# Performance work log

Measured on AMD Instinct MI355X. Metric: run time of the kernel, lower is better.

Reference implementation:

```python
import jax, jax.numpy as jnp
import numpy as np

D = 768; H = 12; DH = D // H; L = 12; FF = 3072; P = 20
IMG = (640, 360); NP_ = (IMG[0] // P) * (IMG[1] // P)  # 576 patches
NC = 10
EPS = 1e-5


def setup_inputs() -> dict:
    key = jax.random.key(0)
    ks = jax.random.split(key, 20)
    s = 0.02
    inp = {
        "x": jax.random.normal(ks[0], (16, 3, IMG[0], IMG[1]), jnp.float32),
        "patch_w": jax.random.normal(ks[1], (D, 3, P, P), jnp.float32) * s,
        "patch_b": jnp.zeros((D,), jnp.float32),
        "pos_emb": jax.random.normal(ks[2], (1, NP_, D), jnp.float32),
        "ln_g": jnp.ones((D,), jnp.float32),
        "ln_b": jnp.zeros((D,), jnp.float32),
        "Wq": jax.random.normal(ks[3], (L, D, D), jnp.float32) * s,
        "bq": jnp.zeros((L, D), jnp.float32),
        "Wk": jax.random.normal(ks[4], (L, D, D), jnp.float32) * s,
        "bk": jnp.zeros((L, D), jnp.float32),
        "Wv": jax.random.normal(ks[5], (L, D, D), jnp.float32) * s,
        "bv": jnp.zeros((L, D), jnp.float32),
        "Wo": jax.random.normal(ks[6], (L, D, D), jnp.float32) * s,
        "bo": jnp.zeros((L, D), jnp.float32),
        "W1": jax.random.normal(ks[7], (L, FF, D), jnp.float32) * s,
        "b1": jnp.zeros((L, FF), jnp.float32),
        "W2": jax.random.normal(ks[8], (L, D, FF), jnp.float32) * s,
        "b2": jnp.zeros((L, D), jnp.float32),
        "fc_w": jax.random.normal(ks[9], (NC, D), jnp.float32) * s,
        "fc_b": jnp.zeros((NC,), jnp.float32),
    }
    return inp


def _layer_norm(x, g, b):
    mu = jnp.mean(x, axis=-1, keepdims=True)
    var = jnp.mean(jnp.square(x - mu), axis=-1, keepdims=True)
    return (x - mu) * jax.lax.rsqrt(var + EPS) * g + b


def _forward(x, patch_w, patch_b, pos_emb, ln_g, ln_b,
             Wq, bq, Wk, bk, Wv, bv, Wo, bo, W1, b1, W2, b2, fc_w, fc_b):
    B = x.shape[0]
    Hp, Wp = IMG[0] // P, IMG[1] // P
    # patch embed: stride=kernel conv == per-patch linear
    patches = x.reshape(B, 3, Hp, P, Wp, P).transpose(0, 2, 4, 1, 3, 5)
    patches = patches.reshape(B, Hp * Wp, 3 * P * P)           # [B, N, 3*p*p]
    h = patches @ patch_w.reshape(D, -1).T + patch_b            # [B, N, D]
    h = h + pos_emb
    h = _layer_norm(h, ln_g, ln_b)

    def layer(h, p):
        wq, bq_, wk, bk_, wv, bv_, wo, bo_, w1, b1_, w2, b2_ = p
        N = h.shape[1]
        def heads(t):  # [B,N,D] -> [B,H,N,DH]
            return t.reshape(B, N, H, DH).transpose(0, 2, 1, 3)
        q = heads(h @ wq.T + bq_)
        k = heads(h @ wk.T + bk_)
        v = heads(h @ wv.T + bv_)
        scores = jnp.einsum('bhqd,bhkd->bhqk', q, k) / jnp.sqrt(jnp.float32(DH))
        attn = jax.nn.softmax(scores, axis=-1)
        o = jnp.einsum('bhqk,bhkd->bhqd', attn, v)
        o = o.transpose(0, 2, 1, 3).reshape(B, N, D) @ wo.T + bo_
        h = h + o
        ff = jax.nn.relu(h @ w1.T + b1_) @ w2.T + b2_
        return h + ff, None

    h, _ = jax.lax.scan(layer, h, (Wq, bq, Wk, bk, Wv, bv, Wo, bo, W1, b1, W2, b2))
    pooled = h.mean(axis=1)                                     # [B, D]
    return pooled @ fc_w.T + fc_b                               # [B, NC]


def reference(x, patch_w, patch_b, pos_emb, ln_g, ln_b,
              Wq, bq, Wk, bk, Wv, bv, Wo, bo, W1, b1, W2, b2, fc_w, fc_b):
    return _forward(x, patch_w, patch_b, pos_emb, ln_g, ln_b,
                    Wq, bq, Wk, bk, Wv, bv, Wo, bo, W1, b1, W2, b2, fc_w, fc_b)
```

## Files before the change

### kernel.cpp

```cpp
#include <hip/hip_runtime.h>
#include <stdint.h>
#include <stddef.h>

typedef __attribute__((ext_vector_type(8))) short short8;
typedef __attribute__((ext_vector_type(4))) float f32x4;

#define D_    768
#define HH    12
#define DHEAD 64
#define NP    576
#define BB    16
#define MROWS 9216
#define KPAT  1216
#define SCL   0.18033688011112042f

static __device__ __forceinline__ unsigned short f2bf(float f){
  union { float f; unsigned int u; } v; v.f = f;
  unsigned int u = v.u;
  return (unsigned short)((u + 0x7FFFu + ((u >> 16) & 1u)) >> 16);
}

static __device__ __forceinline__ void gld16(const void* g, void* l){
  __builtin_amdgcn_global_load_lds((const __attribute__((address_space(1))) void*)g,
                                   (__attribute__((address_space(3))) void*)l,
                                   16, 0, 0);
}

static __device__ __forceinline__ void barx(){
  asm volatile("" ::: "memory");
  __builtin_amdgcn_s_barrier();
  asm volatile("" ::: "memory");
}

template<int MF>
__global__ __launch_bounds__(512) void gemm8p(
    const unsigned short* __restrict__ A,
    const unsigned short* __restrict__ W,
    const float* __restrict__ bias,
    const float* __restrict__ pos,
    const float* res,
    float* outf,
    unsigned short* outb,
    int M, int N, int K, int relu)
{
  constexpr int BM = MF * 32;
  constexpr int NV = (MF == 8) ? 8 : 6;
  __shared__ unsigned short sA[4][BM*32];
  __shared__ unsigned short sB[4][256*32];

  const int NB = N >> 8;
  const int nwg = (int)gridDim.x;
  const int wid0 = (int)blockIdx.x;
  const int xcd = wid0 & 7, bidx = wid0 >> 3;
  const int q = nwg >> 3, r = nwg & 7;
  const int wid = (xcd < r ? xcd*(q+1) : r*(q+1) + (xcd-r)*q) + bidx;
  const int mb = wid / NB, nb = wid % NB;
  const int m0 = mb * BM, n0 = nb << 8;
  const int t = threadIdx.x;
  const int w = t >> 6, l = t & 63;
  const int wr = w >> 2, wc = w & 3;
  const int fr = l & 15, fq = l >> 4;

  const int srow = l >> 2;
  const int schk = (l & 3) ^ ((l >> 3) & 3);

  const f32x4 zero = {0.f, 0.f, 0.f, 0.f};
  f32x4 acc[MF][4];
  #pragma unroll
  for (int i = 0; i < MF; ++i)
    #pragma unroll
    for (int j = 0; j < 4; ++j) acc[i][j] = zero;

  const int KT = K >> 6;

  auto stgA = [&](int h){
    #pragma unroll
    for (int i = 0; i < BM/128; ++i){
      const int rb = i*128 + w*16;
      gld16(A + (size_t)(m0 + rb + srow) * K + (h<<5) + (schk<<3),
            &sA[h & 3][rb*32]);
    }
  };
  auto stgB = [&](int h){
    #pragma unroll
    for (int i = 0; i < 2; ++i){
      const int rb = i*128 + w*16;
      gld16(W + (size_t)(n0 + rb + srow) * K + (h<<5) + (schk<<3),
            &sB[h & 3][rb*32]);
    }
  };
  auto rdA = [&](short8* a, int slot, int mh){
    #pragma unroll
    for (int i = 0; i < MF/2; ++i){
      const int R = wr*(MF*16) + (mh*(MF/2) + i)*16 + fr;
      a[i] = *(const short8*)&sA[slot][R*32 + ((fq ^ ((R>>1)&3))<<3)];
    }
  };
  auto rdB = [&](short8* b, int slot){
    #pragma unroll
    for (int i = 0; i < 4; ++i){
      const int C = wc*64 + i*16 + fr;
      b[i] = *(const short8*)&sB[slot][C*32 + ((fq ^ ((C>>1)&3))<<3)];
    }
  };

  stgA(0); stgB(0); stgA(1); stgB(1); stgA(2); stgB(2);
  asm volatile("s_waitcnt vmcnt(%0)" :: "n"(NV) : "memory");
  barx();

  short8 a[MF/2], b[4];
  for (int kt = 0; kt < KT; ++kt){
    const int s0 = (2*kt) & 3, s1 = (2*kt+1) & 3;
    const int h3 = 2*kt + 3, h4 = 2*kt + 4;
    const bool g3 = h3 < 2*KT, g4 = h4 < 2*KT;
    const bool tail = kt >= KT - 2;

    rdA(a, s0, 0); rdB(b, s0);
    if (g3) stgA(h3);
    barx();
    __builtin_amdgcn_s_setprio(1);
    #pragma unroll
    for (int i = 0; i < MF/2; ++i)
      #pragma unroll
      for (int j = 0; j < 4; ++j)
        acc[i][j] = __builtin_amdgcn_mfma_f32_16x16x32_bf16(a[i], b[j], acc[i][j], 0, 0, 0);
    __builtin_amdgcn_s_setprio(0);
    barx();

    rdA(a, s0, 1);
    if (g3) stgB(h3);
    barx();
    __builtin_amdgcn_s_setprio(1);
    #pragma unroll
    for (int i = 0; i < MF/2; ++i)
      #pragma unroll
      for (int j = 0; j < 4; ++j)
        acc[MF/2 + i][j] = __builtin_amdgcn_mfma_f32_16x16x32_bf16(a[i], b[j], acc[MF/2 + i][j], 0, 0, 0);
    __builtin_amdgcn_s_setprio(0);
    if (tail) asm volatile("s_waitcnt vmcnt(0)" ::: "memory");
    else      asm volatile("s_waitcnt vmcnt(%0)" :: "n"(NV) : "memory");
    barx();

    rdA(a, s1, 0); rdB(b, s1);
    if (g4) stgA(h4);
    barx();
    __builtin_amdgcn_s_setprio(1);
    #pragma unroll
    for (int i = 0; i < MF/2; ++i)
      #pragma unroll
      for (int j = 0; j < 4; ++j)
        acc[i][j] = __builtin_amdgcn_mfma_f32_16x16x32_bf16(a[i], b[j], acc[i][j], 0, 0, 0);
    __builtin_amdgcn_s_setprio(0);
    barx();

    rdA(a, s1, 1);
    if (g4) stgB(h4);
    barx();
    __builtin_amdgcn_s_setprio(1);
    #pragma unroll
    for (int i = 0; i < MF/2; ++i)
      #pragma unroll
      for (int j = 0; j < 4; ++j)
        acc[MF/2 + i][j] = __builtin_amdgcn_mfma_f32_16x16x32_bf16(a[i], b[j], acc[MF/2 + i][j], 0, 0, 0);
    __builtin_amdgcn_s_setprio(0);
    if (tail) asm volatile("s_waitcnt vmcnt(0)" ::: "memory");
    else      asm volatile("s_waitcnt vmcnt(%0)" :: "n"(NV) : "memory");
    barx();
  }

  #pragma unroll
  for (int mf = 0; mf < MF; ++mf){
    #pragma unroll
    for (int nf = 0; nf < 4; ++nf){
      #pragma unroll
      for (int rr = 0; rr < 4; ++rr){
        const int row = m0 + wr*(MF*16) + mf*16 + (fq<<2) + rr;
        const int col = n0 + wc*64 + nf*16 + fr;
        float v = acc[mf][nf][rr] + bias[col];
        if (pos)  v += pos[(size_t)(row % NP) * D_ + col];
        if (res)  v += res[(size_t)row * N + col];
        if (relu) v = fmaxf(v, 0.f);
        const size_t idx = (size_t)row * N + col;
        if (outf) outf[idx] = v;
        if (outb) outb[idx] = f2bf(v);
      }
    }
  }
}

__global__ __launch_bounds__(512) void gemm4p(
    const unsigned short* __restrict__ A,
    const unsigned short* __restrict__ W,
    const float* __restrict__ bias,
    const float* __restrict__ pos,
    const float* res,
    float* outf,
    unsigned short* outb,
    int M, int N, int K, int relu)
{
  __shared__ unsigned short sA[4][128*32];
  __shared__ unsigned short sB[4][128*32];
  const int NB = N >> 7;
  const int nwg = (int)gridDim.x;
  const int wid0 = (int)blockIdx.x;
  const int xcd = wid0 & 7, bidx = wid0 >> 3;
  const int q = nwg >> 3, r = nwg & 7;
  const int wid = (xcd < r ? xcd*(q+1) : r*(q+1) + (xcd-r)*q) + bidx;
  const int mb = wid / NB, nb = wid % NB;
  const int m0 = mb << 7, n0 = nb << 7;
  const int t = threadIdx.x;
  const int w = t >> 6, l = t & 63;
  const int wr = w >> 1, wc = w & 1;
  const int fr = l & 15, fq = l >> 4;

  const int srow = l >> 2;
  const int schk = (l & 3) ^ ((l >> 3) & 3);

  const f32x4 zero = {0.f, 0.f, 0.f, 0.f};
  f32x4 acc[2][4];
  #pragma unroll
  for (int i = 0; i < 2; ++i)
    #pragma unroll
    for (int j = 0; j < 4; ++j) acc[i][j] = zero;

  const int P = K >> 5;

  auto stg = [&](int h){
    const int rb = w*16;
    gld16(A + (size_t)(m0 + rb + srow) * K + (h<<5) + (schk<<3), &sA[h & 3][rb*32]);
    gld16(W + (size_t)(n0 + rb + srow) * K + (h<<5) + (schk<<3), &sB[h & 3][rb*32]);
  };

  stg(0); stg(1); stg(2);
  asm volatile("s_waitcnt vmcnt(4)" ::: "memory");
  barx();

  short8 a[2], b[4];
  for (int p = 0; p < P; ++p){
    const int slot = p & 3;
    #pragma unroll
    for (int i = 0; i < 2; ++i){
      const int R = wr*32 + i*16 + fr;
      a[i] = *(const short8*)&sA[slot][R*32 + ((fq ^ ((R>>1)&3))<<3)];
    }
    #pragma unroll
    for (int i = 0; i < 4; ++i){
      const int C = wc*64 + i*16 + fr;
      b[i] = *(const short8*)&sB[slot][C*32 + ((fq ^ ((C>>1)&3))<<3)];
    }
    if (p + 3 < P) stg(p + 3);
    barx();
    __builtin_amdgcn_s_setprio(1);
    #pragma unroll
    for (int i = 0; i < 2; ++i)
      #pragma unroll
      for (int j = 0; j < 4; ++j)
        acc[i][j] = __builtin_amdgcn_mfma_f32_16x16x32_bf16(a[i], b[j], acc[i][j], 0, 0, 0);
    __builtin_amdgcn_s_setprio(0);
    if (p + 1 < P){
      if      (p <= P - 4) asm volatile("s_waitcnt vmcnt(4)" ::: "memory");
      else if (p == P - 3) asm volatile("s_waitcnt vmcnt(2)" ::: "memory");
      else                 asm volatile("s_waitcnt vmcnt(0)" ::: "memory");
      barx();
    }
  }

  #pragma unroll
  for (int mf = 0; mf < 2; ++mf){
    #pragma unroll
    for (int nf = 0; nf < 4; ++nf){
      #pragma unroll
      for (int rr = 0; rr < 4; ++rr){
        const int row = m0 + wr*32 + mf*16 + (fq<<2) + rr;
        const int col = n0 + wc*64 + nf*16 + fr;
        float v = acc[mf][nf][rr] + bias[col];
        if (pos)  v += pos[(size_t)(row % NP) * D_ + col];
        if (res)  v += res[(size_t)row * N + col];
        if (relu) v = fmaxf(v, 0.f);
        const size_t idx = (size_t)row * N + col;
        if (outf) outf[idx] = v;
        if (outb) outb[idx] = f2bf(v);
      }
    }
  }
}

__global__ __launch_bounds__(384) void k_attn(const unsigned short* __restrict__ qkv,
                                              unsigned short* __restrict__ o)
{
  __shared__ unsigned short Kl[2][32*64];
  __shared__ unsigned short Vt[2][64*64];
  const int nwg = (int)gridDim.x;
  int wid = (int)blockIdx.x;
  wid = (wid & 7) * (nwg >> 3) + (wid >> 3);
  const int bh = wid / 3, qs = wid % 3;
  const int b = bh / HH, h = bh % HH;
  const unsigned short* base = qkv + (size_t)b * NP * 2304 + h * DHEAD;
  const int t = threadIdx.x;
  const int w = t >> 6, l = t & 63;
  const int fr = l & 15, fq = l >> 4;
  const int sg = l & 7;
  const int sr = ((w & 3) << 3) + (l >> 3);
  const bool stw = (t < 256);

  short8 qfa[2], qfb[2];
  #pragma unroll
  for (int qt = 0; qt < 2; ++qt){
    const size_t qrow = (size_t)(qs*192 + (qt*6 + w)*16 + fr);
    qfa[qt] = *(const short8*)(base + qrow*2304 + (fq<<3));
    qfb[qt] = *(const short8*)(base + qrow*2304 + 32 + (fq<<3));
  }

  const f32x4 zero = {0.f, 0.f, 0.f, 0.f};
  float mx_[2] = {-1e30f, -1e30f};
  float ls_[2] = {0.f, 0.f};
  f32x4 oa[2][4];
  #pragma unroll
  for (int qt = 0; qt < 2; ++qt)
    #pragma unroll
    for (int nf = 0; nf < 4; ++nf) oa[qt][nf] = zero;

  if (stw){
    gld16(base + 768 + (size_t)sr*2304 + ((sg ^ (sr&7))<<3), &Kl[0][(w&3)*512]);
    short8 vv = *(const short8*)(base + 1536 + (size_t)sr*2304 + (sg<<3));
    asm volatile("s_waitcnt vmcnt(0)" ::: "memory");
    #pragma unroll
    for (int j = 0; j < 8; ++j){
      const int d = sg*8 + j;
      const int off = (d<<7) + ((((sr>>3) ^ j ^ sg) & 7) << 4) + ((sr&7)<<1);
      *(unsigned short*)((char*)&Vt[0][0] + off) = ((const unsigned short*)&vv)[j];
    }
  }
  __syncthreads();

  for (int kt = 0; kt < 18; ++kt){
    const int buf = kt & 1;
    short8 vv;
    const bool st = stw && (kt < 17);
    if (st){
      const int key = (kt+1)*32 + sr;
      gld16(base + 768 + (size_t)key*2304 + ((sg ^ (sr&7))<<3), &Kl[buf^1][(w&3)*512]);
      vv = *(const short8*)(base + 1536 + (size_t)key*2304 + (sg<<3));
    }

    const char* kb = (const char*)&Kl[buf][0];
    const int r0 = fr, r1 = 16 + fr;
    const short8 k00 = *(const short8*)(kb + (r0<<7) + (((fq    ) ^ (r0&7))<<4));
    const short8 k01 = *(const short8*)(kb + (r0<<7) + (((4+fq ) ^ (r0&7))<<4));
    const short8 k10 = *(const short8*)(kb + (r1<<7) + (((fq    ) ^ (r1&7))<<4));
    const short8 k11 = *(const short8*)(kb + (r1<<7) + (((4+fq ) ^ (r1&7))<<4));
    const char* vb = (const char*)&Vt[buf][0];

    #pragma unroll
    for (int qt = 0; qt < 2; ++qt){
      f32x4 s0 = zero, s1 = zero;
      s0 = __builtin_amdgcn_mfma_f32_16x16x32_bf16(k00, qfa[qt], s0, 0, 0, 0);
      s0 = __builtin_amdgcn_mfma_f32_16x16x32_bf16(k01, qfb[qt], s0, 0, 0, 0);
      s1 = __builtin_amdgcn_mfma_f32_16x16x32_bf16(k10, qfa[qt], s1, 0, 0, 0);
      s1 = __builtin_amdgcn_mfma_f32_16x16x32_bf16(k11, qfb[qt], s1, 0, 0, 0);
      float mx = fmaxf(fmaxf(fmaxf(s0[0], s0[1]), fmaxf(s0[2], s0[3])),
                       fmaxf(fmaxf(s1[0], s1[1]), fmaxf(s1[2], s1[3])));
      mx = fmaxf(mx, __shfl_xor(mx, 16));
      mx = fmaxf(mx, __shfl_xor(mx, 32));
      const float mn = fmaxf(mx_[qt], mx * SCL);
      const float fc = exp2f(mx_[qt] - mn);
      const float p0 = exp2f(s0[0]*SCL - mn), p1 = exp2f(s0[1]*SCL - mn);
      const float p2 = exp2f(s0[2]*SCL - mn), p3 = exp2f(s0[3]*SCL - mn);
      const float p4 = exp2f(s1[0]*SCL - mn), p5 = exp2f(s1[1]*SCL - mn);
      const float p6 = exp2f(s1[2]*SCL - mn), p7 = exp2f(s1[3]*SCL - mn);
      float ps = ((p0+p1)+(p2+p3)) + ((p4+p5)+(p6+p7));
      ps += __shfl_xor(ps, 16);
      ps += __shfl_xor(ps, 32);
      ls_[qt] = ls_[qt] * fc + ps;
      mx_[qt] = mn;
      if (!__all(fc == 1.0f)){
        const float fA = __shfl(fc, (fq<<2) + 0);
        const float fB = __shfl(fc, (fq<<2) + 1);
        const float fC = __shfl(fc, (fq<<2) + 2);
        const float fD = __shfl(fc, (fq<<2) + 3);
        #pragma unroll
        for (int nf = 0; nf < 4; ++nf){
          oa[qt][nf][0] *= fA; oa[qt][nf][1] *= fB;
          oa[qt][nf][2] *= fC; oa[qt][nf][3] *= fD;
        }
      }
      unsigned d0, d1, d2, d3;
      asm("v_cvt_pk_bf16_f32 %0, %1, %2" : "=v"(d0) : "v"(p0), "v"(p1));
      asm("v_cvt_pk_bf16_f32 %0, %1, %2" : "=v"(d1) : "v"(p2), "v"(p3));
      asm("v_cvt_pk_bf16_f32 %0, %1, %2" : "=v"(d2) : "v"(p4), "v"(p5));
      asm("v_cvt_pk_bf16_f32 %0, %1, %2" : "=v"(d3) : "v"(p6), "v"(p7));
      const int srcA = fr + ((fq & 1) << 5);
      const unsigned a0 = (unsigned)__shfl((int)d0, srcA);
      const unsigned a1 = (unsigned)__shfl((int)d1, srcA);
      const unsigned a2 = (unsigned)__shfl((int)d2, srcA);
      const unsigned a3 = (unsigned)__shfl((int)d3, srcA);
      const unsigned b0 = (unsigned)__shfl((int)d0, srcA + 16);
      const unsigned b1 = (unsigned)__shfl((int)d1, srcA + 16);
      const unsigned b2 = (unsigned)__shfl((int)d2, srcA + 16);
      const unsigned b3 = (unsigned)__shfl((int)d3, srcA + 16);
      const bool hi = fq >= 2;
      union { unsigned u[4]; short8 v; } pk;
      pk.u[0] = hi ? a2 : a0;
      pk.u[1] = hi ? a3 : a1;
      pk.u[2] = hi ? b2 : b0;
      pk.u[3] = hi ? b3 : b1;
      const short8 pa = pk.v;
      #pragma unroll
      for (int nf = 0; nf < 4; ++nf){
        const int d = (nf<<4) + fr;
        const short8 vf = *(const short8*)(vb + (d<<7) + (((fq ^ (d&7) ^ (d>>3)) & 7)<<4));
        oa[qt][nf] = __builtin_amdgcn_mfma_f32_16x16x32_bf16(pa, vf, oa[qt][nf], 0, 0, 0);
      }
    }

    if (st){
      asm volatile("s_waitcnt vmcnt(0)" ::: "memory");
      #pragma unroll
      for (int j = 0; j < 8; ++j){
        const int d = sg*8 + j;
        const int off = (d<<7) + ((((sr>>3) ^ j ^ sg) & 7) << 4) + ((sr&7)<<1);
        *(unsigned short*)((char*)&Vt[buf^1][0] + off) = ((const unsigned short*)&vv)[j];
      }
    }
    __syncthreads();
  }

  #pragma unroll
  for (int qt = 0; qt < 2; ++qt){
    const float rl = 1.f / ls_[qt];
    const float rA = __shfl(rl, (fq<<2)+0), rB = __shfl(rl, (fq<<2)+1);
    const float rC = __shfl(rl, (fq<<2)+2), rD = __shfl(rl, (fq<<2)+3);
    const size_t r0 = (size_t)(b*NP + qs*192 + (qt*6 + w)*16 + (fq<<2));
    #pragma unroll
    for (int nf = 0; nf < 4; ++nf){
      const int col = h*DHEAD + (nf<<4) + fr;
      o[(r0 + 0)*D_ + col] = f2bf(oa[qt][nf][0] * rA);
      o[(r0 + 1)*D_ + col] = f2bf(oa[qt][nf][1] * rB);
      o[(r0 + 2)*D_ + col] = f2bf(oa[qt][nf][2] * rC);
      o[(r0 + 3)*D_ + col] = f2bf(oa[qt][nf][3] * rD);
    }
  }
}

__global__ void k_f2b(const float* __restrict__ s, unsigned short* __restrict__ d, long n){
  long i = (long)blockIdx.x * blockDim.x + threadIdx.x;
  const long st = (long)gridDim.x * blockDim.x;
  for (; i < n; i += st) d[i] = f2bf(s[i]);
}

__global__ void k_pack_qkvw(const float* __restrict__ Wq, const float* __restrict__ Wk,
                            const float* __restrict__ Wv, unsigned short* __restrict__ dst){
  const long n = (long)12 * 2304 * 768;
  long i = (long)blockIdx.x * blockDim.x + threadIdx.x;
  const long st = (long)gridDim.x * blockDim.x;
  for (; i < n; i += st){
    const int lay = (int)(i / (2304 * 768));
    const int rem = (int)(i % (2304 * 768));
    const int r = rem / 768, k = rem % 768;
    const float* s = (r < 768) ? Wq : ((r < 1536) ? Wk : Wv);
    const int rr = (r < 768) ? r : ((r < 1536) ? r - 768 : r - 1536);
    dst[i] = f2bf(s[(size_t)lay * 589824 + (size_t)rr * 768 + k]);
  }
}

__global__ void k_pack_qkvb(const float* __restrict__ bq, const float* __restrict__ bk,
                            const float* __restrict__ bv, float* __restrict__ dst){
  const int i = blockIdx.x * 256 + threadIdx.x;
  if (i >= 12 * 2304) return;
  const int lay = i / 2304, r = i % 2304;
  const float* s = (r < 768) ? bq : ((r < 1536) ? bk : bv);
  const int rr = (r < 768) ? r : ((r < 1536) ? r - 768 : r - 1536);
  dst[i] = s[lay * 768 + rr];
}

__global__ void k_patchw(const float* __restrict__ s, unsigned short* __restrict__ d){
  const long n = (long)768 * KPAT;
  long i = (long)blockIdx.x * blockDim.x + threadIdx.x;
  const long st = (long)gridDim.x * blockDim.x;
  for (; i < n; i += st){
    const int r = (int)(i / KPAT), k = (int)(i % KPAT);
    d[i] = (k < 1200) ? f2bf(s[(size_t)r * 1200 + k]) : (unsigned short)0;
  }
}

__global__ void k_patches(const float* __restrict__ x, unsigned short* __restrict__ d){
  const long n = (long)MROWS * KPAT;
  long i = (long)blockIdx.x * blockDim.x + threadIdx.x;
  const long st = (long)gridDim.x * blockDim.x;
  for (; i < n; i += st){
    const int mrow = (int)(i / KPAT), k = (int)(i % KPAT);
    unsigned short v = 0;
    if (k < 1200){
      const int c = k / 400, rem = k % 400, py = rem / 20, px = rem % 20;
      const int b = mrow / NP, pn = mrow % NP, hp = pn / 18, wp = pn % 18;
      v = f2bf(x[(((size_t)b * 3 + c) * 640 + hp * 20 + py) * 360 + wp * 20 + px]);
    }
    d[i] = v;
  }
}

__global__ __launch_bounds__(256) void k_ln(float* h, unsigned short* hb,
                                            const float* __restrict__ g,
                                            const float* __restrict__ bt){
  const int r = blockIdx.x, t = threadIdx.x;
  const size_t base = (size_t)r * D_;
  const float x0 = h[base + t], x1 = h[base + t + 256], x2 = h[base + t + 512];
  float s = x0 + x1 + x2;
  #pragma unroll
  for (int o = 1; o < 64; o <<= 1) s += __shfl_xor(s, o);
  __shared__ float red[8];
  const int w = t >> 6, l = t & 63;
  if (l == 0) red[w] = s;
  __syncthreads();
  const float mu = (red[0] + red[1] + red[2] + red[3]) * (1.f / 768.f);
  const float d0 = x0 - mu, d1 = x1 - mu, d2 = x2 - mu;
  float v = d0*d0 + d1*d1 + d2*d2;
  #pragma unroll
  for (int o = 1; o < 64; o <<= 1) v += __shfl_xor(v, o);
  if (l == 0) red[4 + w] = v;
  __syncthreads();
  const float var = (red[4] + red[5] + red[6] + red[7]) * (1.f / 768.f);
  const float rs = rsqrtf(var + 1e-5f);
  const float y0 = d0 * rs * g[t]       + bt[t];
  const float y1 = d1 * rs * g[t + 256] + bt[t + 256];
  const float y2 = d2 * rs * g[t + 512] + bt[t + 512];
  h[base + t] = y0; h[base + t + 256] = y1; h[base + t + 512] = y2;
  hb[base + t] = f2bf(y0); hb[base + t + 256] = f2bf(y1); hb[base + t + 512] = f2bf(y2);
}

__global__ void k_pool(const float* __restrict__ h, float* __restrict__ p){
  const int i = blockIdx.x * 256 + threadIdx.x;
  const int b = i / D_, c = i % D_;
  const float* base = h + (size_t)b * NP * D_ + c;
  float s = 0.f;
  for (int n = 0; n < NP; ++n) s += base[(size_t)n * D_];
  p[i] = s * (1.f / 576.f);
}

__global__ __launch_bounds__(64) void k_fc(const float* __restrict__ p, const float* __restrict__ w,
                                           const float* __restrict__ bias, float* __restrict__ out){
  const int oi = blockIdx.x;
  const int b = oi / 10, j = oi % 10;
  const int l = threadIdx.x;
  float s = 0.f;
  for (int c = l; c < D_; c += 64) s += p[b * D_ + c] * w[j * D_ + c];
  #pragma unroll
  for (int o = 1; o < 64; o <<= 1) s += __shfl_xor(s, o);
  if (l == 0) out[oi] = s + bias[j];
}

extern "C" void kernel_launch(void* const* d_in, const int* in_sizes, int n_in,
                              void* d_out, int out_size, void* d_ws, size_t ws_size,
                              hipStream_t stream)
{
  const float* x       = (const float*)d_in[0];
  const float* patch_w = (const float*)d_in[1];
  const float* patch_b = (const float*)d_in[2];
  const float* pos_emb = (const float*)d_in[3];
  const float* ln_g    = (const float*)d_in[4];
  const float* ln_b    = (const float*)d_in[5];
  const float* Wq      = (const float*)d_in[6];
  const float* bq      = (const float*)d_in[7];
  const float* Wk      = (const float*)d_in[8];
  const float* bk      = (const float*)d_in[9];
  const float* Wv      = (const float*)d_in[10];
  const float* bv      = (const float*)d_in[11];
  const float* Wo      = (const float*)d_in[12];
  const float* bo      = (const float*)d_in[13];
  const float* W1      = (const float*)d_in[14];
  const float* b1      = (const float*)d_in[15];
  const float* W2      = (const float*)d_in[16];
  const float* b2      = (const float*)d_in[17];
  const float* fc_w    = (const float*)d_in[18];
  const float* fc_b    = (const float*)d_in[19];
  float* out = (float*)d_out;
  (void)in_sizes; (void)n_in; (void)out_size; (void)ws_size;

  char* ws = (char*)d_ws;
  size_t off = 0;
  auto alloc = [&](size_t bytes) -> char* {
    char* p = ws + off;
    off += (bytes + 255) & ~(size_t)255;
    return p;
  };
  unsigned short* wqkv    = (unsigned short*)alloc((size_t)12*2304*768*2);
  unsigned short* wo      = (unsigned short*)alloc((size_t)12*768*768*2);
  unsigned short* w1      = (unsigned short*)alloc((size_t)12*3072*768*2);
  unsigned short* w2      = (unsigned short*)alloc((size_t)12*768*3072*2);
  unsigned short* wp      = (unsigned short*)alloc((size_t)768*KPAT*2);
  float*          bqkv    = (float*)alloc((size_t)12*2304*4);
  unsigned short* patches = (unsigned short*)alloc((size_t)MROWS*KPAT*2);
  float*          hf      = (float*)alloc((size_t)MROWS*D_*4);
  unsigned short* hb      = (unsigned short*)alloc((size_t)MROWS*D_*2);
  unsigned short* qkvb    = (unsigned short*)alloc((size_t)MROWS*2304*2);
  unsigned short* ob      = (unsigned short*)alloc((size_t)MROWS*D_*2);
  unsigned short* ffb     = (unsigned short*)alloc((size_t)MROWS*3072*2);
  float*          pooled  = (float*)alloc((size_t)16*D_*4);

  k_pack_qkvw<<<2048, 256, 0, stream>>>(Wq, Wk, Wv, wqkv);
  k_pack_qkvb<<<(12*2304 + 255)/256, 256, 0, stream>>>(bq, bk, bv, bqkv);
  k_f2b<<<2048, 256, 0, stream>>>(Wo, wo, (long)12*768*768);
  k_f2b<<<2048, 256, 0, stream>>>(W1, w1, (long)12*3072*768);
  k_f2b<<<2048, 256, 0, stream>>>(W2, w2, (long)12*768*3072);
  k_patchw<<<2048, 256, 0, stream>>>(patch_w, wp);
  k_patches<<<2048, 256, 0, stream>>>(x, patches);

  gemm4p<<<72*6, 512, 0, stream>>>(patches, wp, patch_b, pos_emb,
                                   nullptr, hf, nullptr, MROWS, 768, KPAT, 0);
  k_ln<<<MROWS, 256, 0, stream>>>(hf, hb, ln_g, ln_b);

  for (int l = 0; l < 12; ++l){
    gemm8p<8><<<36*9, 512, 0, stream>>>(hb, wqkv + (size_t)l*2304*768, bqkv + l*2304,
                                        nullptr, nullptr, nullptr, qkvb, MROWS, 2304, 768, 0);
    k_attn<<<576, 384, 0, stream>>>(qkvb, ob);
    gemm4p<<<72*6, 512, 0, stream>>>(ob, wo + (size_t)l*768*768, bo + l*768,
                                     nullptr, hf, hf, hb, MROWS, 768, 768, 0);
    gemm8p<8><<<36*12, 512, 0, stream>>>(hb, w1 + (size_t)l*3072*768, b1 + (size_t)l*3072,
                                         nullptr, nullptr, nullptr, ffb, MROWS, 3072, 768, 1);
    gemm4p<<<72*6, 512, 0, stream>>>(ffb, w2 + (size_t)l*768*3072, b2 + l*768,
                                     nullptr, hf, hf, hb, MROWS, 768, 3072, 0);
  }
  k_pool<<<48, 256, 0, stream>>>(hf, pooled);
  k_fc<<<160, 64, 0, stream>>>(pooled, fc_w, fc_b, out);
}
```

Measured before the change: 3.896 ms.

## Replace 256x256 QKV/FF1 GEMM with 256x128 triple-buffered kernel; vectorize conversions

The QKV and FF1 projections now use a new GEMM kernel with 256x128 output tiles. It has a simpler 3-stage LDS ring that loads one 32-wide K slice per step, with a single barrier pair per iteration and launch bounds that allow more blocks per CU. This doubles the grid size and lowers LDS and register use, trading per-tile data reuse for higher occupancy and fewer barriers. The weight and patch conversion kernels are also vectorized to process four floats per thread.

```diff
diff --git a/kernel.cpp b/kernel.cpp
--- a/kernel.cpp
+++ b/kernel.cpp
@@ -4,6 +4,8 @@
 
 typedef __attribute__((ext_vector_type(8))) short short8;
 typedef __attribute__((ext_vector_type(4))) float f32x4;
+typedef __attribute__((ext_vector_type(4))) float float4v;
+typedef __attribute__((ext_vector_type(4))) unsigned short us4;
 
 #define D_    768
 #define HH    12
@@ -20,6 +22,12 @@
   return (unsigned short)((u + 0x7FFFu + ((u >> 16) & 1u)) >> 16);
 }
 
+static __device__ __forceinline__ us4 f2bf4(float4v v){
+  us4 r;
+  r.x = f2bf(v.x); r.y = f2bf(v.y); r.z = f2bf(v.z); r.w = f2bf(v.w);
+  return r;
+}
+
 static __device__ __forceinline__ void gld16(const void* g, void* l){
   __builtin_amdgcn_global_load_lds((const __attribute__((address_space(1))) void*)g,
                                    (__attribute__((address_space(3))) void*)l,
@@ -32,8 +40,7 @@
   asm volatile("" ::: "memory");
 }
 
-template<int MF>
-__global__ __launch_bounds__(512) void gemm8p(
+__global__ __launch_bounds__(512, 4) void gemm3r(
     const unsigned short* __restrict__ A,
     const unsigned short* __restrict__ W,
     const float* __restrict__ bias,
@@ -43,138 +50,83 @@
     unsigned short* outb,
     int M, int N, int K, int relu)
 {
-  constexpr int BM = MF * 32;
-  constexpr int NV = (MF == 8) ? 8 : 6;
-  __shared__ unsigned short sA[4][BM*32];
-  __shared__ unsigned short sB[4][256*32];
-
-  const int NB = N >> 8;
+  __shared__ unsigned short sA[3][256*32];
+  __shared__ unsigned short sB[3][128*32];
+  const int NB = N >> 7;
   const int nwg = (int)gridDim.x;
   const int wid0 = (int)blockIdx.x;
   const int xcd = wid0 & 7, bidx = wid0 >> 3;
   const int q = nwg >> 3, r = nwg & 7;
   const int wid = (xcd < r ? xcd*(q+1) : r*(q+1) + (xcd-r)*q) + bidx;
   const int mb = wid / NB, nb = wid % NB;
-  const int m0 = mb * BM, n0 = nb << 8;
+  const int m0 = mb << 8, n0 = nb << 7;
   const int t = threadIdx.x;
   const int w = t >> 6, l = t & 63;
-  const int wr = w >> 2, wc = w & 3;
+  const int wr = w >> 1, wc = w & 1;
   const int fr = l & 15, fq = l >> 4;
-
   const int srow = l >> 2;
   const int schk = (l & 3) ^ ((l >> 3) & 3);
 
   const f32x4 zero = {0.f, 0.f, 0.f, 0.f};
-  f32x4 acc[MF][4];
-  #pragma unroll
-  for (int i = 0; i < MF; ++i)
+  f32x4 acc[4][4];
+  #pragma unroll
+  for (int i = 0; i < 4; ++i)
     #pragma unroll
     for (int j = 0; j < 4; ++j) acc[i][j] = zero;
 
-  const int KT = K >> 6;
-
-  auto stgA = [&](int h){
-    #pragma unroll
-    for (int i = 0; i < BM/128; ++i){
-      const int rb = i*128 + w*16;
-      gld16(A + (size_t)(m0 + rb + srow) * K + (h<<5) + (schk<<3),
-            &sA[h & 3][rb*32]);
-    }
-  };
-  auto stgB = [&](int h){
+  const int P = K >> 5;
+
+  auto stg = [&](int h){
+    const int s = h % 3;
     #pragma unroll
     for (int i = 0; i < 2; ++i){
       const int rb = i*128 + w*16;
-      gld16(W + (size_t)(n0 + rb + srow) * K + (h<<5) + (schk<<3),
-            &sB[h & 3][rb*32]);
-    }
+      gld16(A + (size_t)(m0 + rb + srow) * K + (h<<5) + (schk<<3), &sA[s][rb*32]);
+    }
+    const int rb = w*16;
+    gld16(W + (size_t)(n0 + rb + srow) * K + (h<<5) + (schk<<3), &sB[s][rb*32]);
   };
-  auto rdA = [&](short8* a, int slot, int mh){
-    #pragma unroll
-    for (int i = 0; i < MF/2; ++i){
-      const int R = wr*(MF*16) + (mh*(MF/2) + i)*16 + fr;
-      a[i] = *(const short8*)&sA[slot][R*32 + ((fq ^ ((R>>1)&3))<<3)];
-    }
-  };
-  auto rdB = [&](short8* b, int slot){
+
+  stg(0); stg(1);
+  asm volatile("s_waitcnt vmcnt(3)" ::: "memory");
+  barx();
+
+  for (int p = 0; p < P; ++p){
+    const int s = p % 3;
+    short8 a[4], b[4];
     #pragma unroll
     for (int i = 0; i < 4; ++i){
-      const int C = wc*64 + i*16 + fr;
-      b[i] = *(const short8*)&sB[slot][C*32 + ((fq ^ ((C>>1)&3))<<3)];
-    }
-  };
-
-  stgA(0); stgB(0); stgA(1); stgB(1); stgA(2); stgB(2);
-  asm volatile("s_waitcnt vmcnt(%0)" :: "n"(NV) : "memory");
-  barx();
-
-  short8 a[MF/2], b[4];
-  for (int kt = 0; kt < KT; ++kt){
-    const int s0 = (2*kt) & 3, s1 = (2*kt+1) & 3;
-    const int h3 = 2*kt + 3, h4 = 2*kt + 4;
-    const bool g3 = h3 < 2*KT, g4 = h4 < 2*KT;
-    const bool tail = kt >= KT - 2;
-
-    rdA(a, s0, 0); rdB(b, s0);
-    if (g3) stgA(h3);
+      const int R = wr*64 + i*16 + fr;
+      a[i] = *(const short8*)&sA[s][R*32 + ((fq ^ ((R>>1)&3))<<3)];
+    }
+    #pragma unroll
+    for (int j = 0; j < 4; ++j){
+      const int C = wc*64 + j*16 + fr;
+      b[j] = *(const short8*)&sB[s][C*32 + ((fq ^ ((C>>1)&3))<<3)];
+    }
+    if (p + 2 < P) stg(p + 2);
     barx();
     __builtin_amdgcn_s_setprio(1);
     #pragma unroll
-    for (int i = 0; i < MF/2; ++i)
+    for (int i = 0; i < 4; ++i)
       #pragma unroll
       for (int j = 0; j < 4; ++j)
         acc[i][j] = __builtin_amdgcn_mfma_f32_16x16x32_bf16(a[i], b[j], acc[i][j], 0, 0, 0);
     __builtin_amdgcn_s_setprio(0);
-    barx();
-
-    rdA(a, s0, 1);
-    if (g3) stgB(h3);
-    barx();
-    __builtin_amdgcn_s_setprio(1);
-    #pragma unroll
-    for (int i = 0; i < MF/2; ++i)
-      #pragma unroll
-      for (int j = 0; j < 4; ++j)
-        acc[MF/2 + i][j] = __builtin_amdgcn_mfma_f32_16x16x32_bf16(a[i], b[j], acc[MF/2 + i][j], 0, 0, 0);
-    __builtin_amdgcn_s_setprio(0);
-    if (tail) asm volatile("s_waitcnt vmcnt(0)" ::: "memory");
-    else      asm volatile("s_waitcnt vmcnt(%0)" :: "n"(NV) : "memory");
-    barx();
-
-    rdA(a, s1, 0); rdB(b, s1);
-    if (g4) stgA(h4);
-    barx();
-    __builtin_amdgcn_s_setprio(1);
-    #pragma unroll
-    for (int i = 0; i < MF/2; ++i)
-      #pragma unroll
-      for (int j = 0; j < 4; ++j)
-        acc[i][j] = __builtin_amdgcn_mfma_f32_16x16x32_bf16(a[i], b[j], acc[i][j], 0, 0, 0);
-    __builtin_amdgcn_s_setprio(0);
-    barx();
-
-    rdA(a, s1, 1);
-    if (g4) stgB(h4);
-    barx();
-    __builtin_amdgcn_s_setprio(1);
-    #pragma unroll
-    for (int i = 0; i < MF/2; ++i)
-      #pragma unroll
-      for (int j = 0; j < 4; ++j)
-        acc[MF/2 + i][j] = __builtin_amdgcn_mfma_f32_16x16x32_bf16(a[i], b[j], acc[MF/2 + i][j], 0, 0, 0);
-    __builtin_amdgcn_s_setprio(0);
-    if (tail) asm volatile("s_waitcnt vmcnt(0)" ::: "memory");
-    else      asm volatile("s_waitcnt vmcnt(%0)" :: "n"(NV) : "memory");
-    barx();
-  }
-
-  #pragma unroll
-  for (int mf = 0; mf < MF; ++mf){
+    if (p + 1 < P){
+      if (p == P - 2) asm volatile("s_waitcnt vmcnt(0)" ::: "memory");
+      else            asm volatile("s_waitcnt vmcnt(3)" ::: "memory");
+      barx();
+    }
+  }
+
+  #pragma unroll
+  for (int mf = 0; mf < 4; ++mf){
     #pragma unroll
     for (int nf = 0; nf < 4; ++nf){
       #pragma unroll
       for (int rr = 0; rr < 4; ++rr){
-        const int row = m0 + wr*(MF*16) + mf*16 + (fq<<2) + rr;
+        const int row = m0 + wr*64 + mf*16 + (fq<<2) + rr;
         const int col = n0 + wc*64 + nf*16 + fr;
         float v = acc[mf][nf][rr] + bias[col];
         if (pos)  v += pos[(size_t)(row % NP) * D_ + col];
@@ -442,24 +394,26 @@
   }
 }
 
-__global__ void k_f2b(const float* __restrict__ s, unsigned short* __restrict__ d, long n){
+__global__ void k_f2b(const float* __restrict__ s, unsigned short* __restrict__ d, long n4){
   long i = (long)blockIdx.x * blockDim.x + threadIdx.x;
   const long st = (long)gridDim.x * blockDim.x;
-  for (; i < n; i += st) d[i] = f2bf(s[i]);
+  for (; i < n4; i += st)
+    ((us4*)d)[i] = f2bf4(((const float4v*)s)[i]);
 }
 
 __global__ void k_pack_qkvw(const float* __restrict__ Wq, const float* __restrict__ Wk,
                             const float* __restrict__ Wv, unsigned short* __restrict__ dst){
-  const long n = (long)12 * 2304 * 768;
+  const long n4 = (long)12 * 2304 * 192;
   long i = (long)blockIdx.x * blockDim.x + threadIdx.x;
   const long st = (long)gridDim.x * blockDim.x;
-  for (; i < n; i += st){
-    const int lay = (int)(i / (2304 * 768));
-    const int rem = (int)(i % (2304 * 768));
-    const int r = rem / 768, k = rem % 768;
+  for (; i < n4; i += st){
+    const int lay = (int)(i / (2304 * 192));
+    const int rem = (int)(i % (2304 * 192));
+    const int r = rem / 192, k4 = rem % 192;
     const float* s = (r < 768) ? Wq : ((r < 1536) ? Wk : Wv);
     const int rr = (r < 768) ? r : ((r < 1536) ? r - 768 : r - 1536);
-    dst[i] = f2bf(s[(size_t)lay * 589824 + (size_t)rr * 768 + k]);
+    const float4v v = *(const float4v*)(s + (size_t)lay * 589824 + (size_t)rr * 768 + k4*4);
+    ((us4*)dst)[i] = f2bf4(v);
   }
 }
 
@@ -474,28 +428,33 @@
 }
 
 __global__ void k_patchw(const float* __restrict__ s, unsigned short* __restrict__ d){
-  const long n = (long)768 * KPAT;
+  const long n4 = (long)768 * (KPAT/4);
   long i = (long)blockIdx.x * blockDim.x + threadIdx.x;
   const long st = (long)gridDim.x * blockDim.x;
-  for (; i < n; i += st){
-    const int r = (int)(i / KPAT), k = (int)(i % KPAT);
-    d[i] = (k < 1200) ? f2bf(s[(size_t)r * 1200 + k]) : (unsigned short)0;
+  for (; i < n4; i += st){
+    const int r = (int)(i / (KPAT/4)), k4 = (int)(i % (KPAT/4));
+    us4 o = {0,0,0,0};
+    if (k4*4 < 1200)
+      o = f2bf4(*(const float4v*)(s + (size_t)r * 1200 + k4*4));
+    ((us4*)d)[i] = o;
   }
 }
 
 __global__ void k_patches(const float* __restrict__ x, unsigned short* __restrict__ d){
-  const long n = (long)MROWS * KPAT;
+  const long n4 = (long)MROWS * (KPAT/4);
   long i = (long)blockIdx.x * blockDim.x + threadIdx.x;
   const long st = (long)gridDim.x * blockDim.x;
-  for (; i < n; i += st){
-    const int mrow = (int)(i / KPAT), k = (int)(i % KPAT);
-    unsigned short v = 0;
+  for (; i < n4; i += st){
+    const int mrow = (int)(i / (KPAT/4)), k4 = (int)(i % (KPAT/4));
+    const int k = k4 * 4;
+    us4 o = {0,0,0,0};
     if (k < 1200){
       const int c = k / 400, rem = k % 400, py = rem / 20, px = rem % 20;
       const int b = mrow / NP, pn = mrow % NP, hp = pn / 18, wp = pn % 18;
-      v = f2bf(x[(((size_t)b * 3 + c) * 640 + hp * 20 + py) * 360 + wp * 20 + px]);
-    }
-    d[i] = v;
+      const float4v v = *(const float4v*)(x + ((((size_t)b * 3 + c) * 640 + hp * 20 + py) * 360 + wp * 20 + px));
+      o = f2bf4(v);
+    }
+    ((us4*)d)[i] = o;
   }
 }
 
@@ -599,9 +558,9 @@
 
   k_pack_qkvw<<<2048, 256, 0, stream>>>(Wq, Wk, Wv, wqkv);
   k_pack_qkvb<<<(12*2304 + 255)/256, 256, 0, stream>>>(bq, bk, bv, bqkv);
-  k_f2b<<<2048, 256, 0, stream>>>(Wo, wo, (long)12*768*768);
-  k_f2b<<<2048, 256, 0, stream>>>(W1, w1, (long)12*3072*768);
-  k_f2b<<<2048, 256, 0, stream>>>(W2, w2, (long)12*768*3072);
+  k_f2b<<<2048, 256, 0, stream>>>(Wo, wo, (long)12*768*768/4);
+  k_f2b<<<2048, 256, 0, stream>>>(W1, w1, (long)12*3072*768/4);
+  k_f2b<<<2048, 256, 0, stream>>>(W2, w2, (long)12*768*3072/4);
   k_patchw<<<2048, 256, 0, stream>>>(patch_w, wp);
   k_patches<<<2048, 256, 0, stream>>>(x, patches);
 
@@ -610,13 +569,13 @@
   k_ln<<<MROWS, 256, 0, stream>>>(hf, hb, ln_g, ln_b);
 
   for (int l = 0; l < 12; ++l){
-    gemm8p<8><<<36*9, 512, 0, stream>>>(hb, wqkv + (size_t)l*2304*768, bqkv + l*2304,
-                                        nullptr, nullptr, nullptr, qkvb, MROWS, 2304, 768, 0);
+    gemm3r<<<36*18, 512, 0, stream>>>(hb, wqkv + (size_t)l*2304*768, bqkv + l*2304,
+                                      nullptr, nullptr, nullptr, qkvb, MROWS, 2304, 768, 0);
     k_attn<<<576, 384, 0, stream>>>(qkvb, ob);
     gemm4p<<<72*6, 512, 0, stream>>>(ob, wo + (size_t)l*768*768, bo + l*768,
                                      nullptr, hf, hf, hb, MROWS, 768, 768, 0);
-    gemm8p<8><<<36*12, 512, 0, stream>>>(hb, w1 + (size_t)l*3072*768, b1 + (size_t)l*3072,
-                                         nullptr, nullptr, nullptr, ffb, MROWS, 3072, 768, 1);
+    gemm3r<<<36*24, 512, 0, stream>>>(hb, w1 + (size_t)l*3072*768, b1 + (size_t)l*3072,
+                                      nullptr, nullptr, nullptr, ffb, MROWS, 3072, 768, 1);
     gemm4p<<<72*6, 512, 0, stream>>>(ffb, w2 + (size_t)l*768*3072, b2 + l*768,
                                      nullptr, hf, hf, hb, MROWS, 768, 3072, 0);
   }
```

New measurement: 3.544 ms. 1.1x faster.
